# Kernel tuning notes

Measured on AMD Instinct MI355X. Metric: run time of the kernel, lower is better.

## Reference

```python
import jax, jax.numpy as jnp
import numpy as np

HID = 2048
HEAD = 64
NH = HID // HEAD  # 32 heads
B, T = 4, 2048


def setup_inputs() -> dict:
    key = jax.random.key(0)
    ks = jax.random.split(key, 32)
    def n(i, shape, sc):
        return (jax.random.normal(ks[i], shape, jnp.float32) * sc).astype(jnp.float32)
    return {
        "hidden": n(0, (B, T, HID), 1.0),
        "attn_x": n(1, (B, HID), 1.0),
        "attn_kv": n(2, (B, NH, HEAD, HEAD), 0.1),
        "ffn_x": n(3, (B, HID), 1.0),
        "time_maa_x": n(4, (1, 1, HID), 0.5),
        "time_maa_w": n(5, (1, 1, HID), 0.5),
        "time_maa_k": n(6, (1, 1, HID), 0.5),
        "time_maa_v": n(7, (1, 1, HID), 0.5),
        "time_maa_r": n(8, (1, 1, HID), 0.5),
        "time_maa_g": n(9, (1, 1, HID), 0.5),
        "time_maa_w1": n(10, (HID, 160), 0.02),
        "time_maa_w2": n(11, (5, 32, HID), 0.02),
        "time_decay": n(12, (1, 1, HID), 0.5),
        "time_decay_w1": n(13, (HID, 64), 0.02),
        "time_decay_w2": n(14, (64, HID), 0.02),
        "time_faaaa": n(15, (NH, HEAD), 0.5),
        "receptance_w": n(16, (HID, HID), 0.02),
        "key_w": n(17, (HID, HID), 0.02),
        "value_w": n(18, (HID, HID), 0.02),
        "gate_w": n(19, (HID, HID), 0.02),
        "output_w": n(20, (HID, HID), 0.02),
        "gn_gamma": 1.0 + n(21, (HID,), 0.1),
        "gn_beta": n(22, (HID,), 0.1),
    }


def reference(hidden, attn_x, attn_kv, ffn_x,
              time_maa_x, time_maa_w, time_maa_k, time_maa_v, time_maa_r, time_maa_g,
              time_maa_w1, time_maa_w2, time_decay, time_decay_w1, time_decay_w2,
              time_faaaa, receptance_w, key_w, value_w, gate_w, output_w,
              gn_gamma, gn_beta):
    Bb, Tt, C = hidden.shape
    x = hidden
    shifted = jnp.concatenate([attn_x[:, None, :], x[:, :-1, :]], axis=1)
    dx = shifted - x
    time_mix = x + dx * time_maa_x
    # token-shift LoRA: (B,T,C)@(C,160) -> (5,B*T,32)@(5,32,C) -> five mixes
    xxx = jnp.tanh(time_mix @ time_maa_w1).reshape(Bb * Tt, 5, 32).transpose(1, 0, 2)
    xxx = jnp.einsum('nbk,nkc->nbc', xxx, time_maa_w2)
    mw, mk, mv, mr, mg = xxx.reshape(5, Bb, Tt, C)
    xw = x + dx * (time_maa_w + mw)
    xk = x + dx * (time_maa_k + mk)
    xv = x + dx * (time_maa_v + mv)
    xr = x + dx * (time_maa_r + mr)
    xg = x + dx * (time_maa_g + mg)
    r = (xr @ receptance_w).reshape(Bb, Tt, NH, HEAD).transpose(0, 2, 1, 3)  # (B,H,T,hs)
    k = (xk @ key_w).reshape(Bb, Tt, NH, HEAD).transpose(0, 2, 1, 3)
    v = (xv @ value_w).reshape(Bb, Tt, NH, HEAD).transpose(0, 2, 1, 3)
    g = jax.nn.silu(xg @ gate_w)
    td = time_decay + jnp.tanh(xw @ time_decay_w1) @ time_decay_w2  # (B,T,C)
    w = jnp.exp(-jnp.exp(td)).reshape(Bb, Tt, NH, HEAD).transpose(0, 2, 1, 3)
    # Source updates layer_state only AFTER the time loop, so inside the loop the
    # state is the constant attn_kv:  out_t = r_t @ (u * (k_t v_t^T) + S0).
    rk = jnp.einsum('bhtd,hd,bhtd->bht', r, time_faaaa, k)
    out = rk[..., None] * v + jnp.einsum('bhtd,bhde->bhte', r, attn_kv)  # (B,H,T,hs)
    new_attn_kv = k[:, :, -1, :, None] * v[:, :, -1, None, :] + w[:, :, -1, :, None] * attn_kv
    new_attn_x = hidden[:, -1]
    out = out.transpose(0, 2, 1, 3).reshape(Bb, Tt, C)
    # keras GroupNormalization(groups=NH) on (B,T,C): stats over (T, within-group channels)
    go = out.reshape(Bb, Tt, NH, HEAD)
    mean = go.mean(axis=(1, 3), keepdims=True)
    var = go.var(axis=(1, 3), keepdims=True)
    eps = 1e-5 * HEAD ** 2
    out = ((go - mean) * jax.lax.rsqrt(var + eps)).reshape(Bb, Tt, C) * gn_gamma + gn_beta
    out = (out * g) @ output_w
    return out, new_attn_x, new_attn_kv, ffn_x
```

## Files before the change

kernel.cpp:

```cpp
#include <hip/hip_runtime.h>

#define HID 2048
#define TSEQ 2048
#define BBATCH 4
#define MROWS 8192
#define NHEADS 32

typedef float fvec4 __attribute__((ext_vector_type(4)));
typedef unsigned short usvec4 __attribute__((ext_vector_type(4)));
typedef unsigned short usvec8 __attribute__((ext_vector_type(8)));
typedef __bf16 bh8 __attribute__((ext_vector_type(8)));
typedef float f32x4 __attribute__((ext_vector_type(4)));

__device__ __forceinline__ float bf2f(unsigned short u){
  return __uint_as_float(((unsigned int)u) << 16);
}
__device__ __forceinline__ unsigned short f2bf(float f){
  unsigned int u = __float_as_uint(f);
  return (unsigned short)((u + 0x7fffu + ((u >> 16) & 1u)) >> 16);
}
__device__ __forceinline__ void gll16(const void* g, void* lds){
  __builtin_amdgcn_global_load_lds(
      (const __attribute__((address_space(1))) unsigned int*)g,
      (__attribute__((address_space(3))) unsigned int*)lds, 16, 0, 0);
}

__global__ void tcast_kernel(const float* __restrict__ in, unsigned short* __restrict__ out,
                             int R, int C){
  __shared__ float tile[32][33];
  int c0 = blockIdx.x * 32, r0 = blockIdx.y * 32;
  int tx = threadIdx.x, ty = threadIdx.y;
  for (int i = ty; i < 32; i += 8){
    int r = r0 + i, c = c0 + tx;
    tile[i][tx] = (r < R && c < C) ? in[(size_t)r * C + c] : 0.f;
  }
  __syncthreads();
  for (int i = ty; i < 32; i += 8){
    int c = c0 + i, r = r0 + tx;
    if (c < C && r < R) out[(size_t)c * R + r] = f2bf(tile[tx][i]);
  }
}

__global__ void zero_stats_kernel(float* __restrict__ gsum, float* __restrict__ gsqs){
  int i = threadIdx.x;
  gsum[i] = 0.f;
  gsqs[i] = 0.f;
}

__global__ void tmix_kernel(const float* __restrict__ hidden, const float* __restrict__ attn_x,
                            const float* __restrict__ tmx, unsigned short* __restrict__ tm){
  int i4 = blockIdx.x * 256 + threadIdx.x;
  int row = i4 >> 9;
  int c4 = i4 & 511;
  fvec4 x = *(const fvec4*)&hidden[(size_t)i4 * 4];
  fvec4 p;
  if ((row & (TSEQ - 1)) == 0){
    int b = row >> 11;
    p = *(const fvec4*)&attn_x[b * HID + c4 * 4];
  } else {
    p = *(const fvec4*)&hidden[(size_t)(i4 - 512) * 4];
  }
  fvec4 tx = *(const fvec4*)&tmx[c4 * 4];
  fvec4 t = x + (p - x) * tx;
  usvec4 o;
  o[0]=f2bf(t[0]); o[1]=f2bf(t[1]); o[2]=f2bf(t[2]); o[3]=f2bf(t[3]);
  *(usvec4*)&tm[(size_t)i4 * 4] = o;
}

template<int ACT, int OUTBF16>
__global__ __launch_bounds__(256, 2) void gemm_kernel(
    const unsigned short* __restrict__ A, const unsigned short* __restrict__ Bt,
    void* __restrict__ Cptr, int M, int N, int K, int ldc)
{
  __shared__ unsigned short As[128 * 32];
  __shared__ unsigned short Bs[128 * 32];
  const int tid = threadIdx.x;
  const int lane = tid & 63;
  const int w = tid >> 6;
  const int wr = w >> 1, wc = w & 1;
  const int lr = lane & 15, lq = lane >> 4;
  const int rowBase = blockIdx.y * 128;
  const int colBase = blockIdx.x * 128;

  const int arow = tid >> 2;
  const int ach = tid & 3;
  const unsigned short* aptr0 = A + (size_t)(rowBase + arow) * K + ach * 8;
  const unsigned short* aptr1 = aptr0 + (size_t)64 * K;
  int br0 = colBase + arow;      if (br0 > N - 1) br0 = N - 1;
  int br1 = colBase + arow + 64; if (br1 > N - 1) br1 = N - 1;
  const unsigned short* bptr0 = Bt + (size_t)br0 * K + ach * 8;
  const unsigned short* bptr1 = Bt + (size_t)br1 * K + ach * 8;

  f32x4 acc[4][4] = {};

  const int nk = K >> 5;
  for (int kk = 0; kk < nk; ++kk){
    gll16(aptr0, &As[tid * 8]);
    gll16(aptr1, &As[(tid + 256) * 8]);
    gll16(bptr0, &Bs[tid * 8]);
    gll16(bptr1, &Bs[(tid + 256) * 8]);
    aptr0 += 32; aptr1 += 32; bptr0 += 32; bptr1 += 32;
    __syncthreads();
    bh8 af[4], bfv[4];
    #pragma unroll
    for (int m = 0; m < 4; ++m)
      af[m] = *reinterpret_cast<const bh8*>(&As[(wr * 64 + m * 16 + lr) * 32 + lq * 8]);
    #pragma unroll
    for (int n = 0; n < 4; ++n)
      bfv[n] = *reinterpret_cast<const bh8*>(&Bs[(wc * 64 + n * 16 + lr) * 32 + lq * 8]);
    #pragma unroll
    for (int m = 0; m < 4; ++m)
      #pragma unroll
      for (int n = 0; n < 4; ++n)
        acc[m][n] = __builtin_amdgcn_mfma_f32_16x16x32_bf16(af[m], bfv[n], acc[m][n], 0, 0, 0);
    __syncthreads();
  }

  #pragma unroll
  for (int m = 0; m < 4; ++m){
    int gr0 = rowBase + wr * 64 + m * 16 + lq * 4;
    #pragma unroll
    for (int n = 0; n < 4; ++n){
      int gc = colBase + wc * 64 + n * 16 + lr;
      if (gc < N){
        #pragma unroll
        for (int q = 0; q < 4; ++q){
          float v = acc[m][n][q];
          if constexpr (ACT == 1) v = tanhf(v);
          else if constexpr (ACT == 2) v = v / (1.0f + __expf(-v));
          size_t off = (size_t)(gr0 + q) * ldc + gc;
          if constexpr (OUTBF16) ((unsigned short*)Cptr)[off] = f2bf(v);
          else                   ((float*)Cptr)[off] = v;
        }
      }
    }
  }
}

template<int ACT, int OUTBF16>
__global__ __launch_bounds__(512, 2) void gemm256_kernel(
    const unsigned short* __restrict__ A, const unsigned short* __restrict__ Bt,
    void* __restrict__ Cptr, int K)
{
  __shared__ unsigned short smem[65536];
  const int tid = threadIdx.x;
  const int lane = tid & 63, w = tid >> 6;
  const int wr = w >> 2, wc = w & 3;
  const int lr = lane & 15, lq = lane >> 4;
  const int rowBase = blockIdx.y * 256;
  const int colBase = blockIdx.x * 256;
  const int N = gridDim.x * 256;

  const unsigned short* srcp[8];
  int dstoff[8];
  #pragma unroll
  for (int l = 0; l < 8; ++l){
    int ci = (l & 3) * 512 + tid;
    int r = ci >> 3, c = ci & 7;
    int gchunk = c ^ (r & 7);
    const unsigned short* base = (l < 4) ? A : Bt;
    int grow = ((l < 4) ? rowBase : colBase) + r;
    srcp[l] = base + (size_t)grow * K + gchunk * 8;
    dstoff[l] = ((l < 4) ? 0 : 16384) + ci * 8;
  }

  f32x4 acc[8][4] = {};

  auto STAGE = [&](unsigned short* buf){
    #pragma unroll
    for (int l = 0; l < 8; ++l){
      gll16(srcp[l], buf + dstoff[l]);
      srcp[l] += 64;
    }
  };

  auto COMPUTE = [&](const unsigned short* buf){
    const unsigned short* aB = buf;
    const unsigned short* bB = buf + 16384;
    #pragma unroll
    for (int s = 0; s < 2; ++s){
      bh8 af[8], bf[4];
      #pragma unroll
      for (int m = 0; m < 8; ++m){
        int row = wr * 128 + m * 16 + lr;
        af[m] = *reinterpret_cast<const bh8*>(
            &aB[row * 64 + (((s * 4 + lq) ^ (row & 7)) * 8)]);
      }
      #pragma unroll
      for (int n = 0; n < 4; ++n){
        int row = wc * 64 + n * 16 + lr;
        bf[n] = *reinterpret_cast<const bh8*>(
            &bB[row * 64 + (((s * 4 + lq) ^ (row & 7)) * 8)]);
      }
      #pragma unroll
      for (int m = 0; m < 8; ++m)
        #pragma unroll
        for (int n = 0; n < 4; ++n)
          acc[m][n] = __builtin_amdgcn_mfma_f32_16x16x32_bf16(af[m], bf[n], acc[m][n], 0, 0, 0);
    }
  };

  unsigned short* buf0 = smem;
  unsigned short* buf1 = smem + 32768;

  STAGE(buf0);
  __syncthreads();
  const int nt = K >> 6;
  for (int t = 0; t < nt - 1; ++t){
    unsigned short* cur = (t & 1) ? buf1 : buf0;
    unsigned short* nxt = (t & 1) ? buf0 : buf1;
    STAGE(nxt);
    COMPUTE(cur);
    __syncthreads();
  }
  COMPUTE((nt & 1) ? buf0 : buf1);

  #pragma unroll
  for (int m = 0; m < 8; ++m){
    int gr0 = rowBase + wr * 128 + m * 16 + lq * 4;
    #pragma unroll
    for (int n = 0; n < 4; ++n){
      int gc = colBase + wc * 64 + n * 16 + lr;
      #pragma unroll
      for (int q = 0; q < 4; ++q){
        float v = acc[m][n][q];
        if constexpr (ACT == 1) v = tanhf(v);
        else if constexpr (ACT == 2) v = v / (1.0f + __expf(-v));
        size_t off = (size_t)(gr0 + q) * N + gc;
        if constexpr (OUTBF16) ((unsigned short*)Cptr)[off] = f2bf(v);
        else                   ((float*)Cptr)[off] = v;
      }
    }
  }
}

__global__ __launch_bounds__(256) void mix_kernel(
    const float* __restrict__ xxx, const float* __restrict__ hidden,
    const float* __restrict__ attn_x, const float* __restrict__ w2,
    const float* __restrict__ tmk, const float* __restrict__ tmv,
    const float* __restrict__ tmr, const float* __restrict__ tmg,
    unsigned short* __restrict__ xk, unsigned short* __restrict__ xv,
    unsigned short* __restrict__ xr, unsigned short* __restrict__ xg)
{
  __shared__ __attribute__((aligned(16))) unsigned short smem[20992];
  unsigned short* xs   = smem;
  unsigned short* w2t  = smem + 10752;
  unsigned short* out4 = smem;

  const int tid = threadIdx.x;
  const int r0 = blockIdx.y * 64, c0 = blockIdx.x * 64;
  const int w = tid >> 6, lane = tid & 63, lr = lane & 15, lq = lane >> 4;

  for (int idx = tid; idx < 64 * 40; idx += 256){
    int r = idx / 40, cq = idx - r * 40;
    fvec4 v = *(const fvec4*)&xxx[(size_t)(r0 + r) * 160 + cq * 4];
    usvec4 o;
    o[0]=f2bf(v[0]); o[1]=f2bf(v[1]); o[2]=f2bf(v[2]); o[3]=f2bf(v[3]);
    *(usvec4*)&xs[r * 168 + cq * 4] = o;
  }
  for (int idx = tid; idx < 4 * 32 * 16; idx += 256){
    int n = idx >> 9;
    int rem = idx & 511;
    int j = rem >> 4, cq = rem & 15;
    fvec4 v = *(const fvec4*)&w2[(size_t)((n + 1) * 32 + j) * HID + c0 + cq * 4];
    #pragma unroll
    for (int cc = 0; cc < 4; ++cc)
      w2t[(n * 64 + cq * 4 + cc) * 40 + j] = f2bf(v[cc]);
  }
  __syncthreads();

  f32x4 acc[4][4] = {};
  #pragma unroll
  for (int n = 0; n < 4; ++n){
    bh8 afr = *reinterpret_cast<const bh8*>(&xs[(w * 16 + lr) * 168 + (n + 1) * 32 + lq * 8]);
    #pragma unroll
    for (int ct = 0; ct < 4; ++ct){
      bh8 bfr = *reinterpret_cast<const bh8*>(&w2t[(n * 64 + ct * 16 + lr) * 40 + lq * 8]);
      acc[ct][n] = __builtin_amdgcn_mfma_f32_16x16x32_bf16(afr, bfr, acc[ct][n], 0, 0, 0);
    }
  }
  __syncthreads();

  #pragma unroll
  for (int ct = 0; ct < 4; ++ct){
    int gc = c0 + ct * 16 + lr;
    float tk_ = tmk[gc], tv_ = tmv[gc], tr_ = tmr[gc], tg_ = tmg[gc];
    #pragma unroll
    for (int q = 0; q < 4; ++q){
      int row64 = w * 16 + lq * 4 + q;
      int gr = r0 + row64;
      size_t rowoff = (size_t)gr * HID + gc;
      float xx = hidden[rowoff];
      float pp = ((gr & (TSEQ - 1)) == 0) ? attn_x[(gr >> 11) * HID + gc]
                                          : hidden[rowoff - HID];
      float dxv = pp - xx;
      int lo = row64 * 72 + ct * 16 + lr;
      out4[(0 * 64 * 72) + lo] = f2bf(xx + dxv * (tk_ + acc[ct][0][q]));
      out4[(1 * 64 * 72) + lo] = f2bf(xx + dxv * (tv_ + acc[ct][1][q]));
      out4[(2 * 64 * 72) + lo] = f2bf(xx + dxv * (tr_ + acc[ct][2][q]));
      out4[(3 * 64 * 72) + lo] = f2bf(xx + dxv * (tg_ + acc[ct][3][q]));
    }
  }
  __syncthreads();

  #pragma unroll
  for (int a = 0; a < 4; ++a){
    unsigned short* dst = (a == 0) ? xk : (a == 1) ? xv : (a == 2) ? xr : xg;
    #pragma unroll
    for (int pass = 0; pass < 2; ++pass){
      int row64 = pass * 32 + (tid >> 3);
      int c8 = (tid & 7) * 8;
      usvec8 v8 = *(const usvec8*)&out4[(a * 64 + row64) * 72 + c8];
      *(usvec8*)&dst[(size_t)(r0 + row64) * HID + c0 + c8] = v8;
    }
  }
}

__global__ __launch_bounds__(256) void attn_kernel(
    const unsigned short* __restrict__ rb, const unsigned short* __restrict__ kb,
    const unsigned short* __restrict__ vb, const float* __restrict__ attn_kv,
    const float* __restrict__ faaaa, unsigned short* __restrict__ out0b,
    float* __restrict__ gsum, float* __restrict__ gsqs)
{
  const int bh = blockIdx.y;
  const int b = bh >> 5, h = bh & 31;
  const int tid = threadIdx.x, lane = tid & 63, w = tid >> 6;
  const int lr = lane & 15, lq = lane >> 4;
  const int t0 = blockIdx.x * 256 + w * 64;
  const size_t rowbase = (size_t)(b * TSEQ + t0) * HID + h * 64;

  const float* akvp = attn_kv + (size_t)bh * 4096;
  bh8 bfr[2][4];
  #pragma unroll
  for (int kk = 0; kk < 2; ++kk)
    #pragma unroll
    for (int n = 0; n < 4; ++n)
      #pragma unroll
      for (int j = 0; j < 8; ++j)
        bfr[kk][n][j] = (__bf16)akvp[(kk * 32 + lq * 8 + j) * 64 + n * 16 + lr];

  float fa0[8], fa1[8];
  #pragma unroll
  for (int j = 0; j < 8; ++j){
    fa0[j] = faaaa[h * 64 + lq * 8 + j];
    fa1[j] = faaaa[h * 64 + 32 + lq * 8 + j];
  }

  __shared__ __attribute__((aligned(16))) float rk_s[4][64];
  __shared__ __attribute__((aligned(16))) unsigned short outb[4][64][72];

  f32x4 acc[4][4] = {};
  #pragma unroll
  for (int m = 0; m < 4; ++m){
    size_t ra = rowbase + (size_t)(m * 16 + lr) * HID;
    bh8 a0 = *reinterpret_cast<const bh8*>(&rb[ra + lq * 8]);
    bh8 a1 = *reinterpret_cast<const bh8*>(&rb[ra + 32 + lq * 8]);
    usvec8 k0 = *reinterpret_cast<const usvec8*>(&kb[ra + lq * 8]);
    usvec8 k1 = *reinterpret_cast<const usvec8*>(&kb[ra + 32 + lq * 8]);
    float p = 0.f;
    #pragma unroll
    for (int j = 0; j < 8; ++j){
      p += (float)a0[j] * fa0[j] * bf2f(k0[j]);
      p += (float)a1[j] * fa1[j] * bf2f(k1[j]);
    }
    p += __shfl_xor(p, 16, 64);
    p += __shfl_xor(p, 32, 64);
    if (lq == 0) rk_s[w][m * 16 + lr] = p;
    #pragma unroll
    for (int n = 0; n < 4; ++n){
      acc[m][n] = __builtin_amdgcn_mfma_f32_16x16x32_bf16(a0, bfr[0][n], acc[m][n], 0, 0, 0);
      acc[m][n] = __builtin_amdgcn_mfma_f32_16x16x32_bf16(a1, bfr[1][n], acc[m][n], 0, 0, 0);
    }
  }
  __syncthreads();

  float ssum = 0.f, ssq = 0.f;
  #pragma unroll
  for (int m = 0; m < 4; ++m){
    fvec4 rk4 = *(const fvec4*)&rk_s[w][m * 16 + lq * 4];
    #pragma unroll
    for (int n = 0; n < 4; ++n){
      int col = n * 16 + lr;
      #pragma unroll
      for (int q = 0; q < 4; ++q){
        int row = m * 16 + lq * 4 + q;
        float vv = bf2f(vb[rowbase + (size_t)row * HID + col]);
        float o = acc[m][n][q] + rk4[q] * vv;
        ssum += o; ssq += o * o;
        outb[w][row][col] = f2bf(o);
      }
    }
  }
  __syncthreads();
  #pragma unroll
  for (int pass = 0; pass < 8; ++pass){
    int row = pass * 8 + (lane >> 3);
    int c8 = (lane & 7) * 8;
    usvec8 o8 = *(const usvec8*)&outb[w][row][c8];
    *(usvec8*)&out0b[rowbase + (size_t)row * HID + c8] = o8;
  }
  #pragma unroll
  for (int off2 = 32; off2 > 0; off2 >>= 1){
    ssum += __shfl_xor(ssum, off2, 64);
    ssq  += __shfl_xor(ssq,  off2, 64);
  }
  if (lane == 0){ atomicAdd(&gsum[bh], ssum); atomicAdd(&gsqs[bh], ssq); }
}

__global__ void gn_stats_kernel(const float* __restrict__ gsum, const float* __restrict__ gsqs,
                                float* __restrict__ meaninv){
  int g = threadIdx.x;
  const float n = (float)(TSEQ * 64);
  float mean = gsum[g] / n;
  float var = gsqs[g] / n - mean * mean;
  meaninv[2 * g]     = mean;
  meaninv[2 * g + 1] = rsqrtf(var + 1e-5f * 64.0f * 64.0f);
}

__global__ void ynorm_kernel(const unsigned short* __restrict__ out0b,
                             const unsigned short* __restrict__ gb,
                             const float* __restrict__ meaninv, const float* __restrict__ gamma,
                             const float* __restrict__ beta, unsigned short* __restrict__ yb){
  int i4 = blockIdx.x * 256 + threadIdx.x;
  int row = i4 >> 9, c4 = i4 & 511;
  int b = row >> 11;
  int c = c4 * 4;
  int g = b * 32 + (c >> 6);
  float mean = meaninv[2 * g], inv = meaninv[2 * g + 1];
  usvec4 o4 = *(const usvec4*)&out0b[(size_t)i4 * 4];
  usvec4 gv = *(const usvec4*)&gb[(size_t)i4 * 4];
  fvec4 ga = *(const fvec4*)&gamma[c];
  fvec4 be = *(const fvec4*)&beta[c];
  usvec4 y;
  #pragma unroll
  for (int cc = 0; cc < 4; ++cc){
    float val = ((bf2f(o4[cc]) - mean) * inv * ga[cc] + be[cc]) * bf2f(gv[cc]);
    y[cc] = f2bf(val);
  }
  *(usvec4*)&yb[(size_t)i4 * 4] = y;
}

__global__ void lastrow_mix_kernel(const float* __restrict__ xxx, const float* __restrict__ hidden,
    const float* __restrict__ w2, const float* __restrict__ tmw, const float* __restrict__ tmk,
    const float* __restrict__ tmv, float* __restrict__ xw_l, float* __restrict__ xk_l,
    float* __restrict__ xv_l){
  int b = blockIdx.y;
  int c = blockIdx.x * 256 + threadIdx.x;
  __shared__ float xsr[160];
  int i = b * TSEQ + (TSEQ - 1);
  if (threadIdx.x < 160) xsr[threadIdx.x] = xxx[(size_t)i * 160 + threadIdx.x];
  __syncthreads();
  float mw = 0.f, mk = 0.f, mv = 0.f;
  for (int j = 0; j < 32; ++j){
    mw += xsr[j]      * w2[(size_t)(j)      * HID + c];
    mk += xsr[32 + j] * w2[(size_t)(32 + j) * HID + c];
    mv += xsr[64 + j] * w2[(size_t)(64 + j) * HID + c];
  }
  float x = hidden[(size_t)i * HID + c];
  float prev = hidden[(size_t)(i - 1) * HID + c];
  float dx = prev - x;
  xw_l[b * HID + c] = x + dx * (tmw[c] + mw);
  xk_l[b * HID + c] = x + dx * (tmk[c] + mk);
  xv_l[b * HID + c] = x + dx * (tmv[c] + mv);
}

__global__ void decay1_part_kernel(const float* __restrict__ xw_l, const float* __restrict__ tdw1,
                                   float* __restrict__ dpart){
  int b = blockIdx.y;
  int chunk = blockIdx.x;
  int j = threadIdx.x & 63, sub = threadIdx.x >> 6;
  float s = 0.f;
  int cbase = chunk * 128 + sub * 32;
  for (int r = 0; r < 32; ++r){
    int c = cbase + r;
    s += xw_l[b * HID + c] * tdw1[(size_t)c * 64 + j];
  }
  __shared__ float red[4][64];
  red[sub][j] = s;
  __syncthreads();
  if (sub == 0)
    dpart[((size_t)b * 16 + chunk) * 64 + j] = red[0][j] + red[1][j] + red[2][j] + red[3][j];
}

__global__ void decay1_reduce_kernel(const float* __restrict__ dpart, float* __restrict__ hdec){
  int tid = threadIdx.x;
  int b = tid >> 6, j = tid & 63;
  float s = 0.f;
  #pragma unroll
  for (int chunk = 0; chunk < 16; ++chunk)
    s += dpart[((size_t)b * 16 + chunk) * 64 + j];
  hdec[b * 64 + j] = tanhf(s);
}

__global__ __launch_bounds__(256) void lastrow_kv_part_kernel(
    const float* __restrict__ xk_l, const float* __restrict__ xv_l,
    const float* __restrict__ keyw, const float* __restrict__ valw,
    float* __restrict__ kpart, float* __restrict__ vpart){
  int c = blockIdx.x * 256 + threadIdx.x;
  int chunk = blockIdx.y;
  __shared__ float xs[2][4][128];
  for (int i = threadIdx.x; i < 512; i += 256){
    int b = i >> 7, r = i & 127;
    xs[0][b][r] = xk_l[b * HID + chunk * 128 + r];
    xs[1][b][r] = xv_l[b * HID + chunk * 128 + r];
  }
  __syncthreads();
  float ka[4] = {0,0,0,0}, va[4] = {0,0,0,0};
  for (int r = 0; r < 128; ++r){
    int c2 = chunk * 128 + r;
    float kw = keyw[(size_t)c2 * HID + c];
    float vw = valw[(size_t)c2 * HID + c];
    #pragma unroll
    for (int b = 0; b < 4; ++b){
      ka[b] += xs[0][b][r] * kw;
      va[b] += xs[1][b][r] * vw;
    }
  }
  #pragma unroll
  for (int b = 0; b < 4; ++b){
    kpart[((size_t)chunk * 4 + b) * HID + c] = ka[b];
    vpart[((size_t)chunk * 4 + b) * HID + c] = va[b];
  }
}

__global__ void lastrow_kv_reduce_kernel(
    const float* __restrict__ kpart, const float* __restrict__ vpart,
    const float* __restrict__ hdec, const float* __restrict__ tdw2,
    const float* __restrict__ tdecay, float* __restrict__ klast,
    float* __restrict__ vlast, float* __restrict__ wlast){
  int c = blockIdx.x * 256 + threadIdx.x;
  float ka[4] = {0,0,0,0}, va[4] = {0,0,0,0};
  for (int chunk = 0; chunk < 16; ++chunk){
    #pragma unroll
    for (int b = 0; b < 4; ++b){
      ka[b] += kpart[((size_t)chunk * 4 + b) * HID + c];
      va[b] += vpart[((size_t)chunk * 4 + b) * HID + c];
    }
  }
  float tdc = tdecay[c];
  float td[4] = {tdc, tdc, tdc, tdc};
  for (int j = 0; j < 64; ++j){
    float w2v = tdw2[(size_t)j * HID + c];
    #pragma unroll
    for (int b = 0; b < 4; ++b) td[b] += hdec[b * 64 + j] * w2v;
  }
  #pragma unroll
  for (int b = 0; b < 4; ++b){
    klast[b * HID + c] = ka[b];
    vlast[b * HID + c] = va[b];
    wlast[b * HID + c] = expf(-expf(td[b]));
  }
}

__global__ void newkv_kernel(const float* __restrict__ klast, const float* __restrict__ vlast,
    const float* __restrict__ wlast, const float* __restrict__ attn_kv,
    float* __restrict__ outkv){
  int idx = blockIdx.x * 256 + threadIdx.x;
  int b = idx >> 17;
  int h = (idx >> 12) & 31;
  int d = (idx >> 6) & 63;
  int e = idx & 63;
  float kl = klast[b * HID + h * 64 + d];
  float vl = vlast[b * HID + h * 64 + e];
  float wl = wlast[b * HID + h * 64 + d];
  outkv[idx] = kl * vl + wl * attn_kv[idx];
}

__global__ void copies_kernel(const float* __restrict__ hidden, const float* __restrict__ ffnx,
                              float* __restrict__ out_attnx, float* __restrict__ out_ffnx){
  int i = blockIdx.x * 256 + threadIdx.x;
  if (i < BBATCH * HID){
    int b = i >> 11, c = i & 2047;
    out_attnx[i] = hidden[((size_t)(b * TSEQ + TSEQ - 1)) * HID + c];
    out_ffnx[i] = ffnx[i];
  }
}

extern "C" void kernel_launch(void* const* d_in, const int* in_sizes, int n_in,
                              void* d_out, int out_size, void* d_ws, size_t ws_size,
                              hipStream_t stream)
{
  (void)in_sizes; (void)n_in; (void)out_size;
  const float* hidden = (const float*)d_in[0];
  const float* attn_x = (const float*)d_in[1];
  const float* attn_kv = (const float*)d_in[2];
  const float* ffn_x = (const float*)d_in[3];
  const float* tmaa_x = (const float*)d_in[4];
  const float* tmaa_w = (const float*)d_in[5];
  const float* tmaa_k = (const float*)d_in[6];
  const float* tmaa_v = (const float*)d_in[7];
  const float* tmaa_r = (const float*)d_in[8];
  const float* tmaa_g = (const float*)d_in[9];
  const float* w1 = (const float*)d_in[10];
  const float* w2 = (const float*)d_in[11];
  const float* tdecay = (const float*)d_in[12];
  const float* tdw1 = (const float*)d_in[13];
  const float* tdw2 = (const float*)d_in[14];
  const float* faaaa = (const float*)d_in[15];
  const float* recw = (const float*)d_in[16];
  const float* keyw = (const float*)d_in[17];
  const float* valw = (const float*)d_in[18];
  const float* gatew = (const float*)d_in[19];
  const float* outw = (const float*)d_in[20];
  const float* gamma = (const float*)d_in[21];
  const float* beta = (const float*)d_in[22];

  float* out_main  = (float*)d_out;
  float* out_attnx = out_main + (size_t)16777216;
  float* out_kv    = out_attnx + 8192;
  float* out_ffn   = out_kv + 524288;

  unsigned short* wr_t = (unsigned short*)d_out;
  unsigned short* wk_t = wr_t + (size_t)4194304;
  unsigned short* wv_t = wk_t + (size_t)4194304;
  unsigned short* wg_t = wv_t + (size_t)4194304;
  unsigned short* out0b = (unsigned short*)d_out;

  char* ws = (char*)d_ws;
  size_t off = 0;
  auto alloc = [&](size_t bytes) -> void* {
    void* p = ws + off; off += (bytes + 255) & ~(size_t)255; return p;
  };
  unsigned short* wo_t = (unsigned short*)alloc(2048ull * 2048 * 2);
  unsigned short* w1_t = (unsigned short*)alloc(160ull * 2048 * 2);
  float* xxx           = (float*)alloc((size_t)MROWS * 160 * 4);
  unsigned short* bufA = (unsigned short*)alloc((size_t)MROWS * HID * 2);
  unsigned short* bufB = (unsigned short*)alloc((size_t)MROWS * HID * 2);
  unsigned short* bufC = (unsigned short*)alloc((size_t)MROWS * HID * 2);
  unsigned short* bufD = (unsigned short*)alloc((size_t)MROWS * HID * 2);
  unsigned short* bufE = (unsigned short*)alloc((size_t)MROWS * HID * 2);
  float* gsum    = (float*)alloc(128 * 4);
  float* gsqs    = (float*)alloc(128 * 4);
  float* meaninv = (float*)alloc(256 * 4);
  float* xw_l  = (float*)alloc(BBATCH * HID * 4);
  float* xk_l  = (float*)alloc(BBATCH * HID * 4);
  float* xv_l  = (float*)alloc(BBATCH * HID * 4);
  float* klast = (float*)alloc(BBATCH * HID * 4);
  float* vlast = (float*)alloc(BBATCH * HID * 4);
  float* wlast = (float*)alloc(BBATCH * HID * 4);
  float* hdec  = (float*)alloc(BBATCH * 64 * 4);
  float* kpart = (float*)alloc(16ull * BBATCH * HID * 4);
  float* vpart = (float*)alloc(16ull * BBATCH * HID * 4);
  float* dpart = (float*)alloc((size_t)BBATCH * 16 * 64 * 4);

  if (off > ws_size) return;

  unsigned short* tm = bufA;
  unsigned short* xg = bufA;
  unsigned short* xr = bufB;
  unsigned short* kb = bufB;
  unsigned short* yb = bufB;
  unsigned short* xk = bufC;
  unsigned short* vb = bufC;
  unsigned short* xv = bufD;
  unsigned short* gb = bufD;
  unsigned short* rb = bufE;

  dim3 tb(32, 8);
  tcast_kernel<<<dim3(64, 64), tb, 0, stream>>>(recw,  wr_t, 2048, 2048);
  tcast_kernel<<<dim3(64, 64), tb, 0, stream>>>(keyw,  wk_t, 2048, 2048);
  tcast_kernel<<<dim3(64, 64), tb, 0, stream>>>(valw,  wv_t, 2048, 2048);
  tcast_kernel<<<dim3(64, 64), tb, 0, stream>>>(gatew, wg_t, 2048, 2048);
  tcast_kernel<<<dim3(64, 64), tb, 0, stream>>>(outw,  wo_t, 2048, 2048);
  tcast_kernel<<<dim3(5, 64),  tb, 0, stream>>>(w1,    w1_t, 2048, 160);
  zero_stats_kernel<<<1, 128, 0, stream>>>(gsum, gsqs);

  tmix_kernel<<<16384, 256, 0, stream>>>(hidden, attn_x, tmaa_x, tm);

  gemm_kernel<1, 0><<<dim3(2, 64), 256, 0, stream>>>(tm, w1_t, xxx, MROWS, 160, HID, 160);

  mix_kernel<<<dim3(32, 128), 256, 0, stream>>>(xxx, hidden, attn_x, w2,
      tmaa_k, tmaa_v, tmaa_r, tmaa_g, xk, xv, xr, xg);

  gemm256_kernel<0, 1><<<dim3(8, 32), 512, 0, stream>>>(xr, wr_t, rb, HID);
  gemm256_kernel<0, 1><<<dim3(8, 32), 512, 0, stream>>>(xk, wk_t, kb, HID);
  gemm256_kernel<0, 1><<<dim3(8, 32), 512, 0, stream>>>(xv, wv_t, vb, HID);
  gemm256_kernel<2, 1><<<dim3(8, 32), 512, 0, stream>>>(xg, wg_t, gb, HID);

  attn_kernel<<<dim3(8, 128), 256, 0, stream>>>(rb, kb, vb, attn_kv, faaaa,
                                                out0b, gsum, gsqs);
  gn_stats_kernel<<<1, 128, 0, stream>>>(gsum, gsqs, meaninv);
  ynorm_kernel<<<16384, 256, 0, stream>>>(out0b, gb, meaninv, gamma, beta, yb);

  gemm256_kernel<0, 0><<<dim3(8, 32), 512, 0, stream>>>(yb, wo_t, out_main, HID);

  lastrow_mix_kernel<<<dim3(8, 4), 256, 0, stream>>>(xxx, hidden, w2, tmaa_w, tmaa_k, tmaa_v,
                                                     xw_l, xk_l, xv_l);
  decay1_part_kernel<<<dim3(16, 4), 256, 0, stream>>>(xw_l, tdw1, dpart);
  decay1_reduce_kernel<<<1, 256, 0, stream>>>(dpart, hdec);
  lastrow_kv_part_kernel<<<dim3(8, 16), 256, 0, stream>>>(xk_l, xv_l, keyw, valw, kpart, vpart);
  lastrow_kv_reduce_kernel<<<8, 256, 0, stream>>>(kpart, vpart, hdec, tdw2, tdecay,
                                                  klast, vlast, wlast);
  newkv_kernel<<<2048, 256, 0, stream>>>(klast, vlast, wlast, attn_kv, out_kv);
  copies_kernel<<<32, 256, 0, stream>>>(hidden, ffn_x, out_attnx, out_ffn);
}
```

Baseline: 706.9 us.

## Deepen gemm256 pipeline to 4-stage K=32 ring with partial vmcnt waits

The 256x256 GEMM now works on K slices of 32 instead of 64 and keeps four LDS buffers, with three stages in flight. Each step waits with a partial s_waitcnt vmcnt plus a barrier rather than draining all loads, so global-to-LDS copies overlap the MFMA work. The change also adds an XCD-aware block remap to improve L2 locality, raises wave priority during the MFMA burst, and uses a new LDS swizzle sized for 32-wide rows. The risk is more barriers per unit of K and hand-written wait counts that have to match the exact number of loads issued per stage.

```diff
diff --git a/kernel.cpp b/kernel.cpp
--- a/kernel.cpp
+++ b/kernel.cpp
@@ -24,6 +24,10 @@
       (const __attribute__((address_space(1))) unsigned int*)g,
       (__attribute__((address_space(3))) unsigned int*)lds, 16, 0, 0);
 }
+
+#define PIPE_SYNC(NSTR)                                              \
+  asm volatile("s_waitcnt vmcnt(" NSTR ")\n\ts_barrier" ::: "memory"); \
+  __builtin_amdgcn_sched_barrier(0);
 
 __global__ void tcast_kernel(const float* __restrict__ in, unsigned short* __restrict__ out,
                              int R, int C){
@@ -147,73 +151,72 @@
   const int lane = tid & 63, w = tid >> 6;
   const int wr = w >> 2, wc = w & 3;
   const int lr = lane & 15, lq = lane >> 4;
-  const int rowBase = blockIdx.y * 256;
-  const int colBase = blockIdx.x * 256;
+
+  const int bid = blockIdx.y * gridDim.x + blockIdx.x;
+  const int xcd = bid & 7, qq = bid >> 3;
+  const int by = xcd * 4 + (qq >> 3);
+  const int bx = qq & 7;
+  const int rowBase = by * 256;
+  const int colBase = bx * 256;
   const int N = gridDim.x * 256;
 
-  const unsigned short* srcp[8];
-  int dstoff[8];
-  #pragma unroll
-  for (int l = 0; l < 8; ++l){
-    int ci = (l & 3) * 512 + tid;
-    int r = ci >> 3, c = ci & 7;
-    int gchunk = c ^ (r & 7);
-    const unsigned short* base = (l < 4) ? A : Bt;
-    int grow = ((l < 4) ? rowBase : colBase) + r;
-    srcp[l] = base + (size_t)grow * K + gchunk * 8;
-    dstoff[l] = ((l < 4) ? 0 : 16384) + ci * 8;
+  const unsigned short* srcA[2]; const unsigned short* srcB[2];
+  int dstA[2], dstB[2];
+  #pragma unroll
+  for (int l = 0; l < 2; ++l){
+    int ci = l * 512 + tid;
+    int r = ci >> 2, c = ci & 3;
+    int g = c ^ ((r >> 1) & 3);
+    srcA[l] = A  + (size_t)(rowBase + r) * K + g * 8;
+    srcB[l] = Bt + (size_t)(colBase + r) * K + g * 8;
+    dstA[l] = ci * 8;
+    dstB[l] = 8192 + ci * 8;
   }
 
   f32x4 acc[8][4] = {};
-
-  auto STAGE = [&](unsigned short* buf){
-    #pragma unroll
-    for (int l = 0; l < 8; ++l){
-      gll16(srcp[l], buf + dstoff[l]);
-      srcp[l] += 64;
+  const int ksel = (lq ^ ((lr >> 1) & 3)) * 8;
+
+  auto STAGE = [&](int t, int bi){
+    unsigned short* buf = smem + bi * 16384;
+    #pragma unroll
+    for (int l = 0; l < 2; ++l){
+      gll16(srcA[l] + (size_t)t * 32, buf + dstA[l]);
+      gll16(srcB[l] + (size_t)t * 32, buf + dstB[l]);
     }
   };
 
-  auto COMPUTE = [&](const unsigned short* buf){
-    const unsigned short* aB = buf;
-    const unsigned short* bB = buf + 16384;
-    #pragma unroll
-    for (int s = 0; s < 2; ++s){
-      bh8 af[8], bf[4];
+  auto COMPUTE = [&](int bi){
+    const unsigned short* aB = smem + bi * 16384;
+    const unsigned short* bB = aB + 8192;
+    bh8 af[8], bf[4];
+    #pragma unroll
+    for (int m = 0; m < 8; ++m)
+      af[m] = *reinterpret_cast<const bh8*>(&aB[(wr * 128 + m * 16 + lr) * 32 + ksel]);
+    #pragma unroll
+    for (int n = 0; n < 4; ++n)
+      bf[n] = *reinterpret_cast<const bh8*>(&bB[(wc * 64 + n * 16 + lr) * 32 + ksel]);
+    __builtin_amdgcn_s_setprio(1);
+    #pragma unroll
+    for (int m = 0; m < 8; ++m)
       #pragma unroll
-      for (int m = 0; m < 8; ++m){
-        int row = wr * 128 + m * 16 + lr;
-        af[m] = *reinterpret_cast<const bh8*>(
-            &aB[row * 64 + (((s * 4 + lq) ^ (row & 7)) * 8)]);
-      }
-      #pragma unroll
-      for (int n = 0; n < 4; ++n){
-        int row = wc * 64 + n * 16 + lr;
-        bf[n] = *reinterpret_cast<const bh8*>(
-            &bB[row * 64 + (((s * 4 + lq) ^ (row & 7)) * 8)]);
-      }
-      #pragma unroll
-      for (int m = 0; m < 8; ++m)
-        #pragma unroll
-        for (int n = 0; n < 4; ++n)
-          acc[m][n] = __builtin_amdgcn_mfma_f32_16x16x32_bf16(af[m], bf[n], acc[m][n], 0, 0, 0);
-    }
+      for (int n = 0; n < 4; ++n)
+        acc[m][n] = __builtin_amdgcn_mfma_f32_16x16x32_bf16(af[m], bf[n], acc[m][n], 0, 0, 0);
+    __builtin_amdgcn_s_setprio(0);
   };
 
-  unsigned short* buf0 = smem;
-  unsigned short* buf1 = smem + 32768;
-
-  STAGE(buf0);
-  __syncthreads();
-  const int nt = K >> 6;
-  for (int t = 0; t < nt - 1; ++t){
-    unsigned short* cur = (t & 1) ? buf1 : buf0;
-    unsigned short* nxt = (t & 1) ? buf0 : buf1;
-    STAGE(nxt);
-    COMPUTE(cur);
-    __syncthreads();
-  }
-  COMPUTE((nt & 1) ? buf0 : buf1);
+  const int nt = K >> 5;
+  STAGE(0, 0); STAGE(1, 1); STAGE(2, 2);
+  PIPE_SYNC("8");
+  for (int t = 0; t < nt - 3; ++t){
+    STAGE(t + 3, (t + 3) & 3);
+    COMPUTE(t & 3);
+    PIPE_SYNC("8");
+  }
+  COMPUTE((nt - 3) & 3);
+  PIPE_SYNC("4");
+  COMPUTE((nt - 2) & 3);
+  PIPE_SYNC("0");
+  COMPUTE((nt - 1) & 3);
 
   #pragma unroll
   for (int m = 0; m < 8; ++m){
```

Result: no change. 695.9 us (-1.6%).
